# Optimization experiments

Measured on AMD Instinct MI355X. Metric: run time of the kernel, lower is better.

Reference implementation:

```python
import jax, jax.numpy as jnp
import numpy as np

CONNECTIONS = {0: [1, 7], 1: [0, 2], 2: [1, 3], 3: [2], 4: [0, 5], 5: [4, 6], 6: [5], 7: [0, 8], 8: [7, 9, 11, 14], 9: [8, 10], 10: [9], 11: [8, 12], 12: [11, 13], 13: [12], 14: [8, 15], 15: [14, 16], 16: [15]}
J = 17
DIM_IN = 128
DIM_OUT = 128
B, T = 64, 243


def _build_bases():
    A1 = np.zeros((J, J), dtype=np.float32)
    for i, neigh in CONNECTIONS.items():
        for j in neigh:
            A1[i, j] = 1.0
            A1[j, i] = 1.0
    eye = np.eye(J, dtype=np.float32)
    adj1_base = A1 + eye
    paths2 = (A1 @ A1 > 0).astype(np.float32)
    adj2_base = ((paths2 - A1 - eye) > 0).astype(np.float32)
    return jnp.asarray(adj1_base), jnp.asarray(adj2_base)


def setup_inputs() -> dict:
    key = jax.random.key(0)
    ks = jax.random.split(key, 8)
    adj1_base, adj2_base = _build_bases()
    # xavier_uniform with gain 1.414 for W
    bound_w = 1.414 * np.sqrt(6.0 / (DIM_IN + DIM_OUT))
    W = jax.random.uniform(ks[0], (DIM_IN, DIM_OUT), jnp.float32, -bound_w, bound_w)
    bound_b = 1.0 / np.sqrt(DIM_IN)
    b = jax.random.uniform(ks[1], (DIM_OUT,), jnp.float32, -bound_b, bound_b)
    return {
        "x": jax.random.normal(ks[2], (B, T, J, DIM_IN), jnp.float32),
        "W": W,
        "b": b,
        "adj_l1": jnp.zeros((J, J), jnp.float32),
        "adj_l2": jnp.zeros((J, J), jnp.float32),
        "w1": jnp.ones((1,), jnp.float32),
        "w2": jnp.ones((1,), jnp.float32),
        "gate_w": jax.random.normal(ks[3], (DIM_IN, 1), jnp.float32) / np.sqrt(DIM_IN),
        "gate_b": jnp.zeros((1,), jnp.float32),
        "bn_gamma": jnp.ones((DIM_OUT,), jnp.float32),
        "bn_beta": jnp.zeros((DIM_OUT,), jnp.float32),
        "adj1_base": adj1_base,
        "adj2_base": adj2_base,
    }


def reference(x, W, b, adj_l1, adj_l2, w1, w2, gate_w, gate_b, bn_gamma, bn_beta, adj1_base, adj2_base):
    Bb, Tt, Jj, C = x.shape
    xf = x.reshape(Bb * Tt, Jj, C)  # (N, J, C)

    # learnable-weighted static adjacency (symmetrized)
    A1w = adj1_base + jax.nn.sigmoid(adj_l1)
    A2w = adj2_base + jax.nn.sigmoid(adj_l2)
    comb = jax.nn.softplus(w1[0]) * A1w + jax.nn.softplus(w2[0]) * A2w
    comb = 0.5 * (comb + comb.T)  # (J, J)

    # dynamic cosine-similarity adjacency
    nrm = jnp.linalg.norm(xf, axis=-1, keepdims=True)
    xn = xf / jnp.maximum(nrm, 1e-12)
    dyn = jax.nn.relu(jnp.einsum("nic,njc->nij", xn, xn)) + jnp.eye(Jj, dtype=x.dtype)

    gate = jax.nn.sigmoid(xf @ gate_w + gate_b)  # (N, J, 1)
    A = gate * comb[None] + (1.0 - gate) * dyn  # (N, J, J)

    # symmetric degree normalization
    deg = A.sum(-1)  # (N, J)
    d = (deg + 1e-6) ** -0.5
    A_hat = d[:, :, None] * A * d[:, None, :]

    h = jnp.einsum("nij,njc->nic", A_hat, xf @ W) + b  # (N, J, dim_out)

    # BatchNorm1d over channels (training-mode batch stats over N and J)
    mean = h.mean(axis=(0, 1))
    var = h.var(axis=(0, 1))
    h = (h - mean) * jax.lax.rsqrt(var + 1e-5) * bn_gamma + bn_beta

    h = jax.nn.relu(h)
    h = h + xf  # residual (dim_in == dim_out -> identity projection)
    return h.reshape(Bb, Tt, Jj, -1)
```

## Files before the change

### kernel.cpp

```cpp
#include <hip/hip_runtime.h>

typedef unsigned short u16;
typedef unsigned int   u32;
typedef __attribute__((ext_vector_type(8))) short bfrag8;
typedef __attribute__((ext_vector_type(4))) float f32x4;

#define NSAMP  15552
#define GRID_B 3888
#define GRID_G 4131

__device__ __forceinline__ u32 bfr(float f){
  u32 u = __float_as_uint(f);
  return (u + 0x7FFFu + ((u >> 16) & 1u)) >> 16;
}
__device__ __forceinline__ u32 packbf(float lo, float hi){
  return bfr(lo) | (bfr(hi) << 16);
}
__device__ __forceinline__ float ubf(u32 v){ return __uint_as_float(v << 16); }
__device__ __forceinline__ float ubfh(u32 v){ return __uint_as_float(v & 0xFFFF0000u); }
__device__ __forceinline__ float sigm(float v){ return 1.0f / (1.0f + __expf(-v)); }
__device__ __forceinline__ float softp(float v){ return (v > 20.f) ? v : log1pf(__expf(v)); }

__global__ void kA(const float* __restrict__ W, const float* __restrict__ al1,
                   const float* __restrict__ al2, const float* __restrict__ w1,
                   const float* __restrict__ w2, const float* __restrict__ a1b,
                   const float* __restrict__ a2b, u16* __restrict__ wt,
                   float* __restrict__ comb, float* __restrict__ mid){
  int idx = blockIdx.x * 256 + threadIdx.x;
  int k = idx >> 7, n = idx & 127;
  wt[n * 128 + k] = (u16)bfr(W[idx]);
  if (blockIdx.x == 1) mid[threadIdx.x] = 0.f;
  if (blockIdx.x == 0){
    float s1 = softp(w1[0]);
    float s2 = softp(w2[0]);
    for (int p = threadIdx.x; p < 289; p += 256){
      int i = p / 17, j = p - i * 17;
      float mij = s1 * (a1b[i*17+j] + sigm(al1[i*17+j])) + s2 * (a2b[i*17+j] + sigm(al2[i*17+j]));
      float mji = s1 * (a1b[j*17+i] + sigm(al1[j*17+i])) + s2 * (a2b[j*17+i] + sigm(al2[j*17+i]));
      comb[i*20 + j] = 0.5f * (mij + mji);
    }
  }
}

struct __align__(16) QSmem { u16 xb[4][18][136]; };
__global__ __launch_bounds__(256, 4) void kQ(const float* __restrict__ x,
    const float* __restrict__ gw, const float* __restrict__ gb,
    float* __restrict__ gbuf){
  __shared__ QSmem q;
  const int tid = threadIdx.x;
  const int w  = tid >> 6;
  const int l  = tid & 63;
  const int g4 = l >> 4;
  const int lc = l & 15;
  const int s  = blockIdx.x * 4 + w;
  const float* xs = x + (size_t)s * 2176;

  float2 g2 = *(const float2*)(gw + 2*l);
  *(u32*)&q.xb[w][17][2*l] = packbf(g2.x, g2.y);
  #pragma unroll
  for (int j = 0; j < 17; j++){
    float2 v = *(const float2*)(xs + j*128 + 2*l);
    *(u32*)&q.xb[w][j][2*l] = packbf(v.x, v.y);
  }
  __syncthreads();
  __builtin_amdgcn_sched_barrier(0);

  const int rB = 16 + ((lc < 2) ? lc : 1);
  f32x4 z4 = {0.f,0.f,0.f,0.f};
  f32x4 dg00 = z4, dg01 = z4, dg11 = z4;
  #pragma unroll
  for (int ks = 0; ks < 4; ks++){
    const int ko = ks*32 + (g4 << 3);
    bfrag8 a0 = *(const bfrag8*)&q.xb[w][lc][ko];
    bfrag8 a1 = *(const bfrag8*)&q.xb[w][rB][ko];
    dg00 = __builtin_amdgcn_mfma_f32_16x16x32_bf16(a0, a0, dg00, 0,0,0);
    dg01 = __builtin_amdgcn_mfma_f32_16x16x32_bf16(a0, a1, dg01, 0,0,0);
    dg11 = __builtin_amdgcn_mfma_f32_16x16x32_bf16(a1, a1, dg11, 0,0,0);
  }
  float* gs = gbuf + (size_t)s * 384;
  const float gbv = gb[0];
  #pragma unroll
  for (int r = 0; r < 4; r++){
    const int i = (g4 << 2) + r;
    gs[i*20 + lc] = dg00[r];
    if (lc == 0){ gs[i*20 + 16] = dg01[r]; gs[16*20 + i] = dg01[r]; }
    if (lc == 1){ gs[360 + i] = sigm(dg01[r] + gbv); }
  }
  if ((lc >> 2) == g4){
    float v = dg00[lc & 3];
    gs[340 + lc] = 1.0f / fmaxf(sqrtf(v), 1e-12f);
  }
  if (l == 0) gs[340 + 16] = 1.0f / fmaxf(sqrtf(dg11[0]), 1e-12f);
  if (l == 1) gs[360 + 16] = sigm(dg11[0] + gbv);
}

struct WaveMem {
  float G[17][20];
  float scr[64];
};
struct BSmem {
  WaveMem wm[4];
  float   combs[340];
};
static_assert(sizeof(BSmem) <= 81920, "LDS budget");

template<int ZOUT>
__device__ __forceinline__ void kBl_body(
    const float* __restrict__ x, const float* __restrict__ combg,
    const float* __restrict__ gbuf, float* __restrict__ out,
    u16* __restrict__ zbuf){
  __shared__ BSmem sm;
  const int tid = threadIdx.x;
  const int w  = tid >> 6;
  const int l  = tid & 63;
  const int g4 = l >> 4;
  const int lc = l & 15;

  for (int p = tid; p < 340; p += 256) sm.combs[p] = combg[p];

  WaveMem& M = sm.wm[w];
  float* Mf = (float*)&M.G[0][0];
  const int s = blockIdx.x * 4 + w;
  const float* gs = gbuf + (size_t)s * 384;
  for (int p = l; p < 380; p += 64) Mf[p] = gs[p];

  const float* xs = x + (size_t)s * 2176;
  float2 xr[17];
  #pragma unroll
  for (int j = 0; j < 17; j++) xr[j] = *(const float2*)(xs + j*128 + 2*l);
  __syncthreads();

  const float iv16 = M.scr[16], gt16 = M.scr[36];
  const float ivj  = M.scr[lc];
  float av00[4], av01[4], dp0[4];
  #pragma unroll
  for (int r = 0; r < 4; r++){
    const int i0 = (g4 << 2) + r;
    const float iv0 = M.scr[i0], gi0 = M.scr[20 + i0];
    float dyn = (i0 == lc) ? 2.0f : fmaxf(M.G[i0][lc] * iv0 * ivj, 0.f);
    av00[r] = gi0 * sm.combs[i0*20 + lc] + (1.f - gi0) * dyn;
    float dyn16 = fmaxf(M.G[i0][16] * iv0 * iv16, 0.f);
    float a16 = gi0 * sm.combs[i0*20 + 16] + (1.f - gi0) * dyn16;
    av01[r] = (lc == 0) ? a16 : 0.f;
    dp0[r] = av00[r] + av01[r];
  }
  float dyn10 = fmaxf(M.G[16][lc] * iv16 * ivj, 0.f);
  float av10 = gt16 * sm.combs[16*20 + lc] + (1.f - gt16) * dyn10;
  float av11 = (lc == 0) ? (gt16 * sm.combs[16*20 + 16] + (1.f - gt16) * 2.0f) : 0.f;
  float dp1 = av10 + av11;
  #pragma unroll
  for (int m = 1; m <= 8; m <<= 1){
    #pragma unroll
    for (int r = 0; r < 4; r++) dp0[r] += __shfl_xor(dp0[r], m, 64);
    dp1 += __shfl_xor(dp1, m, 64);
  }
  float dd0[4];
  #pragma unroll
  for (int r = 0; r < 4; r++) dd0[r] = rsqrtf(dp0[r] + 1e-6f);
  float dd1 = rsqrtf(dp1 + 1e-6f);
  if (lc == 0){
    #pragma unroll
    for (int r = 0; r < 4; r++) M.scr[40 + (g4<<2) + r] = dd0[r];
  }
  if (l == 0) M.scr[40 + 16] = dd1;
  __syncthreads();

  const float dj0 = M.scr[40 + lc];
  const float dj1 = M.scr[40 + 16];
  #pragma unroll
  for (int r = 0; r < 4; r++){
    const int i0 = (g4 << 2) + r;
    M.G[i0][lc] = dd0[r] * av00[r] * dj0;
    if (lc == 0) M.G[i0][16] = dd0[r] * av01[r] * dj1;
  }
  if (g4 == 0) M.G[16][lc] = dd1 * av10 * dj0;
  if (l == 0)  M.G[16][16] = dd1 * av11 * dj1;
  __syncthreads();

  float* ob = out + (size_t)s * 2176;
  u16*   zb = zbuf + (size_t)s * 2176;
  for (int i = 0; i < 17; i++){
    const float4 a0 = *(const float4*)&M.G[i][0];
    const float4 a1 = *(const float4*)&M.G[i][4];
    const float4 a2 = *(const float4*)&M.G[i][8];
    const float4 a3 = *(const float4*)&M.G[i][12];
    const float a16 = M.G[i][16];
    float zx = a0.x*xr[0].x,  zy = a0.x*xr[0].y;
    zx += a0.y*xr[1].x;  zy += a0.y*xr[1].y;
    zx += a0.z*xr[2].x;  zy += a0.z*xr[2].y;
    zx += a0.w*xr[3].x;  zy += a0.w*xr[3].y;
    zx += a1.x*xr[4].x;  zy += a1.x*xr[4].y;
    zx += a1.y*xr[5].x;  zy += a1.y*xr[5].y;
    zx += a1.z*xr[6].x;  zy += a1.z*xr[6].y;
    zx += a1.w*xr[7].x;  zy += a1.w*xr[7].y;
    zx += a2.x*xr[8].x;  zy += a2.x*xr[8].y;
    zx += a2.y*xr[9].x;  zy += a2.y*xr[9].y;
    zx += a2.z*xr[10].x; zy += a2.z*xr[10].y;
    zx += a2.w*xr[11].x; zy += a2.w*xr[11].y;
    zx += a3.x*xr[12].x; zy += a3.x*xr[12].y;
    zx += a3.y*xr[13].x; zy += a3.y*xr[13].y;
    zx += a3.z*xr[14].x; zy += a3.z*xr[14].y;
    zx += a3.w*xr[15].x; zy += a3.w*xr[15].y;
    zx += a16*xr[16].x;  zy += a16*xr[16].y;
    if (ZOUT == 1){
      *(u32*)&zb[i*128 + 2*l] = packbf(zx, zy);
    } else {
      float2 zv; zv.x = zx; zv.y = zy;
      *(float2*)&ob[i*128 + 2*l] = zv;
    }
  }
}

__global__ __launch_bounds__(256, 4) void kBl2(
    const float* __restrict__ x, const float* __restrict__ combg,
    const float* __restrict__ gbuf, u16* __restrict__ zbuf){
  kBl_body<1>(x, combg, gbuf, nullptr, zbuf);
}
__global__ __launch_bounds__(256, 4) void kBl(
    const float* __restrict__ x, const float* __restrict__ combg,
    const float* __restrict__ gbuf, float* __restrict__ out){
  kBl_body<0>(x, combg, gbuf, out, nullptr);
}

__global__ __launch_bounds__(256, 4) void kBf(
    const float* __restrict__ x, const float* __restrict__ gw,
    const float* __restrict__ gb, const float* __restrict__ combg,
    float* __restrict__ out){
  __shared__ BSmem sm;
  const int tid = threadIdx.x;
  const int w  = tid >> 6;
  const int l  = tid & 63;
  const int g4 = l >> 4;
  const int lc = l & 15;

  for (int p = tid; p < 340; p += 256) sm.combs[p] = combg[p];
  __syncthreads();

  WaveMem& M = sm.wm[w];
  float2 g2 = *(const float2*)(gw + 2*l);
  const float gbv = gb[0];
  const int s = blockIdx.x * 4 + w;
  const float* xs = x + (size_t)s * 2176;
  float2 xr[17];
  #pragma unroll
  for (int j = 0; j < 17; j++) xr[j] = *(const float2*)(xs + j*128 + 2*l);

  #pragma unroll
  for (int i = 0; i < 17; i++){
    float p[17];
    #pragma unroll
    for (int j = i; j < 17; j++)
      p[j-i] = xr[i].x*xr[j].x + xr[i].y*xr[j].y;
    float pg = xr[i].x*g2.x + xr[i].y*g2.y;
    #pragma unroll
    for (int m = 1; m <= 32; m <<= 1){
      #pragma unroll
      for (int j = i; j < 17; j++) p[j-i] += __shfl_xor(p[j-i], m, 64);
      pg += __shfl_xor(pg, m, 64);
    }
    #pragma unroll
    for (int j = i; j < 17; j++){
      if (l == j) M.G[i][j] = p[j-i];
      if (i != j && l == i) M.G[j][i] = p[j-i];
    }
    if (l == i){
      M.scr[i]      = 1.0f / fmaxf(sqrtf(p[0]), 1e-12f);
      M.scr[20 + i] = sigm(pg + gbv);
    }
  }
  __syncthreads();

  const float iv16 = M.scr[16], gt16 = M.scr[36];
  const float ivj  = M.scr[lc];
  float av00[4], av01[4], dp0[4];
  #pragma unroll
  for (int r = 0; r < 4; r++){
    const int i0 = (g4 << 2) + r;
    const float iv0 = M.scr[i0], gi0 = M.scr[20 + i0];
    float dyn = (i0 == lc) ? 2.0f : fmaxf(M.G[i0][lc] * iv0 * ivj, 0.f);
    av00[r] = gi0 * sm.combs[i0*20 + lc] + (1.f - gi0) * dyn;
    float dyn16 = fmaxf(M.G[i0][16] * iv0 * iv16, 0.f);
    float a16 = gi0 * sm.combs[i0*20 + 16] + (1.f - gi0) * dyn16;
    av01[r] = (lc == 0) ? a16 : 0.f;
    dp0[r] = av00[r] + av01[r];
  }
  float dyn10 = fmaxf(M.G[16][lc] * iv16 * ivj, 0.f);
  float av10 = gt16 * sm.combs[16*20 + lc] + (1.f - gt16) * dyn10;
  float av11 = (lc == 0) ? (gt16 * sm.combs[16*20 + 16] + (1.f - gt16) * 2.0f) : 0.f;
  float dp1 = av10 + av11;
  #pragma unroll
  for (int m = 1; m <= 8; m <<= 1){
    #pragma unroll
    for (int r = 0; r < 4; r++) dp0[r] += __shfl_xor(dp0[r], m, 64);
    dp1 += __shfl_xor(dp1, m, 64);
  }
  float dd0[4];
  #pragma unroll
  for (int r = 0; r < 4; r++) dd0[r] = rsqrtf(dp0[r] + 1e-6f);
  float dd1 = rsqrtf(dp1 + 1e-6f);
  if (lc == 0){
    #pragma unroll
    for (int r = 0; r < 4; r++) M.scr[40 + (g4<<2) + r] = dd0[r];
  }
  if (l == 0) M.scr[40 + 16] = dd1;
  __syncthreads();

  const float dj0 = M.scr[40 + lc];
  const float dj1 = M.scr[40 + 16];
  #pragma unroll
  for (int r = 0; r < 4; r++){
    const int i0 = (g4 << 2) + r;
    M.G[i0][lc] = dd0[r] * av00[r] * dj0;
    if (lc == 0) M.G[i0][16] = dd0[r] * av01[r] * dj1;
  }
  if (g4 == 0) M.G[16][lc] = dd1 * av10 * dj0;
  if (l == 0)  M.G[16][16] = dd1 * av11 * dj1;
  __syncthreads();

  float* ob = out + (size_t)s * 2176;
  for (int i = 0; i < 17; i++){
    const float4 a0 = *(const float4*)&M.G[i][0];
    const float4 a1 = *(const float4*)&M.G[i][4];
    const float4 a2 = *(const float4*)&M.G[i][8];
    const float4 a3 = *(const float4*)&M.G[i][12];
    const float a16 = M.G[i][16];
    float zx = a0.x*xr[0].x,  zy = a0.x*xr[0].y;
    zx += a0.y*xr[1].x;  zy += a0.y*xr[1].y;
    zx += a0.z*xr[2].x;  zy += a0.z*xr[2].y;
    zx += a0.w*xr[3].x;  zy += a0.w*xr[3].y;
    zx += a1.x*xr[4].x;  zy += a1.x*xr[4].y;
    zx += a1.y*xr[5].x;  zy += a1.y*xr[5].y;
    zx += a1.z*xr[6].x;  zy += a1.z*xr[6].y;
    zx += a1.w*xr[7].x;  zy += a1.w*xr[7].y;
    zx += a2.x*xr[8].x;  zy += a2.x*xr[8].y;
    zx += a2.y*xr[9].x;  zy += a2.y*xr[9].y;
    zx += a2.z*xr[10].x; zy += a2.z*xr[10].y;
    zx += a2.w*xr[11].x; zy += a2.w*xr[11].y;
    zx += a3.x*xr[12].x; zy += a3.x*xr[12].y;
    zx += a3.y*xr[13].x; zy += a3.y*xr[13].y;
    zx += a3.z*xr[14].x; zy += a3.z*xr[14].y;
    zx += a3.w*xr[15].x; zy += a3.w*xr[15].y;
    zx += a16*xr[16].x;  zy += a16*xr[16].y;
    float2 zv; zv.x = zx; zv.y = zy;
    *(float2*)&ob[i*128 + 2*l] = zv;
  }
}

struct __align__(16) G4Smem {
  float hb[4][16][132];
  float stash[4][256];
};
__global__ __launch_bounds__(256, 4) void kG4(const u16* __restrict__ wtg,
    u16* __restrict__ zbuf, float* __restrict__ part){
  __shared__ G4Smem g;
  const int tid = threadIdx.x;
  const int w  = tid >> 6;
  const int l  = tid & 63;
  const int g4 = l >> 4;
  const int lc = l & 15;
  const int R = blockIdx.x * 64 + w * 16;

  const u16* zr = zbuf + (size_t)R * 128;
  f32x4 zero4 = {0.f,0.f,0.f,0.f};
  f32x4 acc[8];
  #pragma unroll
  for (int nf = 0; nf < 8; nf++) acc[nf] = zero4;
  #pragma unroll
  for (int ks = 0; ks < 4; ks++){
    const int ko = ks*32 + (g4 << 3);
    bfrag8 za = *(const bfrag8*)&zr[lc * 128 + ko];
    #pragma unroll
    for (int nf = 0; nf < 8; nf++){
      bfrag8 bw = *(const bfrag8*)&wtg[(nf*16 + lc)*128 + ko];
      acc[nf] = __builtin_amdgcn_mfma_f32_16x16x32_bf16(za, bw, acc[nf], 0,0,0);
    }
  }

  float s[8], q[8];
  #pragma unroll
  for (int nf = 0; nf < 8; nf++){
    float ss = 0.f, qq = 0.f;
    #pragma unroll
    for (int r = 0; r < 4; r++){
      float v = acc[nf][r];
      g.hb[w][4*g4 + r][nf*16 + lc] = v;
      ss += v; qq += v*v;
    }
    ss += __shfl_xor(ss, 16, 64); ss += __shfl_xor(ss, 32, 64);
    qq += __shfl_xor(qq, 16, 64); qq += __shfl_xor(qq, 32, 64);
    s[nf] = ss; q[nf] = qq;
  }
  __builtin_amdgcn_sched_barrier(0);

  {
    const int row = l >> 2, seg = l & 3;
    const float* hrow = &g.hb[w][row][seg * 32];
    u16* zw = zbuf + (size_t)(R + row) * 128 + seg * 32;
    #pragma unroll
    for (int k = 0; k < 4; k++){
      float4 a = *(const float4*)&hrow[k*8];
      float4 b = *(const float4*)&hrow[k*8 + 4];
      u32 p0 = packbf(a.x, a.y), p1 = packbf(a.z, a.w);
      u32 p2 = packbf(b.x, b.y), p3 = packbf(b.z, b.w);
      uint4 pv; pv.x = p0; pv.y = p1; pv.z = p2; pv.w = p3;
      *(uint4*)&zw[k*8] = pv;
    }
  }

  if (l < 16){
    #pragma unroll
    for (int nf = 0; nf < 8; nf++){
      g.stash[w][nf*16 + l]       = s[nf];
      g.stash[w][128 + nf*16 + l] = q[nf];
    }
  }
  __syncthreads();
  part[(size_t)blockIdx.x * 256 + tid] =
      g.stash[0][tid] + g.stash[1][tid] + g.stash[2][tid] + g.stash[3][tid];
}

__global__ __launch_bounds__(256) void kC(const float* __restrict__ part,
    float* __restrict__ mid){
  __shared__ float smem[256];
  const int t = threadIdx.x, c = blockIdx.x;
  float acc = 0.f;
  for (int g = t; g < GRID_G; g += 256) acc += part[(size_t)g * 256 + c];
  smem[t] = acc;
  __syncthreads();
  for (int sft = 128; sft > 0; sft >>= 1){
    if (t < sft) smem[t] += smem[t + sft];
    __syncthreads();
  }
  if (t == 0) mid[c] = smem[0];
}

__global__ __launch_bounds__(256, 4) void kG2a(const u16* __restrict__ wtg,
    const u16* __restrict__ zbuf, float* __restrict__ mid, float* __restrict__ out){
  __shared__ float stash[4][256];
  const int tid = threadIdx.x;
  const int w  = tid >> 6;
  const int l  = tid & 63;
  const int g4 = l >> 4;
  const int lc = l & 15;
  const int R = blockIdx.x * 64 + w * 16;

  const u16* zr = zbuf + (size_t)R * 128;
  f32x4 zero4 = {0.f,0.f,0.f,0.f};
  f32x4 acc[8];
  #pragma unroll
  for (int nf = 0; nf < 8; nf++) acc[nf] = zero4;
  #pragma unroll
  for (int ks = 0; ks < 4; ks++){
    const int ko = ks*32 + (g4 << 3);
    bfrag8 za = *(const bfrag8*)&zr[lc * 128 + ko];
    #pragma unroll
    for (int nf = 0; nf < 8; nf++){
      bfrag8 bw = *(const bfrag8*)&wtg[(nf*16 + lc)*128 + ko];
      acc[nf] = __builtin_amdgcn_mfma_f32_16x16x32_bf16(za, bw, acc[nf], 0,0,0);
    }
  }
  float* hg = out + (size_t)R * 128;
  float s[8], q[8];
  #pragma unroll
  for (int nf = 0; nf < 8; nf++){
    float ss = 0.f, qq = 0.f;
    #pragma unroll
    for (int r = 0; r < 4; r++){
      float v = acc[nf][r];
      hg[(4*g4 + r)*128 + nf*16 + lc] = v;
      ss += v; qq += v*v;
    }
    ss += __shfl_xor(ss, 16, 64); ss += __shfl_xor(ss, 32, 64);
    qq += __shfl_xor(qq, 16, 64); qq += __shfl_xor(qq, 32, 64);
    s[nf] = ss; q[nf] = qq;
  }
  if (l < 16){
    #pragma unroll
    for (int nf = 0; nf < 8; nf++){
      stash[w][nf*16 + l]       = s[nf];
      stash[w][128 + nf*16 + l] = q[nf];
    }
  }
  __syncthreads();
  atomicAdd(&mid[tid], stash[0][tid] + stash[1][tid] + stash[2][tid] + stash[3][tid]);
}

struct __align__(16) GSmem {
  u16 wl[128][132];
  u16 zl[4][16][132];
};
__global__ __launch_bounds__(256, 3) void kG(const u16* __restrict__ wtg,
    float* __restrict__ mid, float* __restrict__ out){
  __shared__ GSmem g;
  const int tid = threadIdx.x;
  const int w  = tid >> 6;
  const int l  = tid & 63;
  const int g4 = l >> 4;
  const int lc = l & 15;

  for (int p = tid; p < 8192; p += 256){
    int n = p >> 6, k2 = (p & 63) * 2;
    *(u32*)&g.wl[n][k2] = ((const u32*)wtg)[p];
  }
  const int R = blockIdx.x * 64 + w * 16;
  float* zg = out + (size_t)R * 128;
  #pragma unroll
  for (int r = 0; r < 16; r++){
    float2 zv = *(const float2*)&zg[r*128 + 2*l];
    *(u32*)&g.zl[w][r][2*l] = packbf(zv.x, zv.y);
  }
  __syncthreads();
  __builtin_amdgcn_sched_barrier(0);

  f32x4 zero4 = {0.f,0.f,0.f,0.f};
  f32x4 acc[8];
  #pragma unroll
  for (int nf = 0; nf < 8; nf++) acc[nf] = zero4;
  #pragma unroll
  for (int ks = 0; ks < 4; ks++){
    const int ko = ks*32 + (g4 << 3);
    bfrag8 za = *(const bfrag8*)&g.zl[w][lc][ko];
    #pragma unroll
    for (int nf = 0; nf < 8; nf++){
      bfrag8 bw = *(const bfrag8*)&g.wl[nf*16 + lc][ko];
      acc[nf] = __builtin_amdgcn_mfma_f32_16x16x32_bf16(za, bw, acc[nf], 0,0,0);
    }
  }

  float s[8], q[8];
  #pragma unroll
  for (int nf = 0; nf < 8; nf++){
    float ss = 0.f, qq = 0.f;
    #pragma unroll
    for (int r = 0; r < 4; r++){
      float v = acc[nf][r];
      zg[(4*g4 + r)*128 + nf*16 + lc] = v;
      ss += v; qq += v*v;
    }
    ss += __shfl_xor(ss, 16, 64); ss += __shfl_xor(ss, 32, 64);
    qq += __shfl_xor(qq, 16, 64); qq += __shfl_xor(qq, 32, 64);
    s[nf] = ss; q[nf] = qq;
  }

  __syncthreads();
  float* stash = (float*)&g.zl[w][0][0];
  if (l < 16){
    #pragma unroll
    for (int nf = 0; nf < 8; nf++){
      stash[nf*16 + l]       = s[nf];
      stash[128 + nf*16 + l] = q[nf];
    }
  }
  __syncthreads();
  float t0 = ((float*)&g.zl[0][0][0])[tid];
  float t1 = ((float*)&g.zl[1][0][0])[tid];
  float t2 = ((float*)&g.zl[2][0][0])[tid];
  float t3 = ((float*)&g.zl[3][0][0])[tid];
  atomicAdd(&mid[tid], t0 + t1 + t2 + t3);
}

__global__ __launch_bounds__(256) void kD2(const float* __restrict__ x,
    const float* __restrict__ mid, const float* __restrict__ gamma,
    const float* __restrict__ beta, const u16* __restrict__ hbuf,
    float* __restrict__ out){
  __shared__ float sc[128], sh[128];
  const int t = threadIdx.x;
  if (t < 128){
    const float ic = 1.0f / 264384.0f;
    float mean = mid[t] * ic;
    float var  = fmaxf(mid[128 + t] * ic - mean*mean, 0.f);
    float scl  = gamma[t] * rsqrtf(var + 1e-5f);
    sc[t] = scl;
    sh[t] = beta[t] - mean * scl;
  }
  __syncthreads();
  const int total16 = 4230144;
  for (int i = blockIdx.x*256 + t; i < total16; i += 2048*256){
    uint4 hv = ((const uint4*)hbuf)[i];
    float4 x0 = ((const float4*)x)[2*i];
    float4 x1 = ((const float4*)x)[2*i + 1];
    int c0 = (i & 15) << 3;
    float4 r0, r1;
    r0.x = fmaxf(ubf (hv.x)*sc[c0+0] + sh[c0+0], 0.f) + x0.x;
    r0.y = fmaxf(ubfh(hv.x)*sc[c0+1] + sh[c0+1], 0.f) + x0.y;
    r0.z = fmaxf(ubf (hv.y)*sc[c0+2] + sh[c0+2], 0.f) + x0.z;
    r0.w = fmaxf(ubfh(hv.y)*sc[c0+3] + sh[c0+3], 0.f) + x0.w;
    r1.x = fmaxf(ubf (hv.z)*sc[c0+4] + sh[c0+4], 0.f) + x1.x;
    r1.y = fmaxf(ubfh(hv.z)*sc[c0+5] + sh[c0+5], 0.f) + x1.y;
    r1.z = fmaxf(ubf (hv.w)*sc[c0+6] + sh[c0+6], 0.f) + x1.z;
    r1.w = fmaxf(ubfh(hv.w)*sc[c0+7] + sh[c0+7], 0.f) + x1.w;
    ((float4*)out)[2*i]     = r0;
    ((float4*)out)[2*i + 1] = r1;
  }
}

__global__ __launch_bounds__(256) void kD(const float* __restrict__ x,
    const float* __restrict__ mid, const float* __restrict__ gamma,
    const float* __restrict__ beta, float* __restrict__ out){
  __shared__ float sc[128], sh[128];
  const int t = threadIdx.x;
  if (t < 128){
    const float ic = 1.0f / 264384.0f;
    float mean = mid[t] * ic;
    float var  = fmaxf(mid[128 + t] * ic - mean*mean, 0.f);
    float scl  = gamma[t] * rsqrtf(var + 1e-5f);
    sc[t] = scl;
    sh[t] = beta[t] - mean * scl;
  }
  __syncthreads();
  const int total = 8460288;
  for (int i = blockIdx.x*256 + t; i < total; i += 2048*256){
    float4 h  = ((const float4*)out)[i];
    float4 xv = ((const float4*)x)[i];
    int c0 = (i & 31) << 2;
    float4 r;
    r.x = fmaxf(h.x*sc[c0+0] + sh[c0+0], 0.f) + xv.x;
    r.y = fmaxf(h.y*sc[c0+1] + sh[c0+1], 0.f) + xv.y;
    r.z = fmaxf(h.z*sc[c0+2] + sh[c0+2], 0.f) + xv.z;
    r.w = fmaxf(h.w*sc[c0+3] + sh[c0+3], 0.f) + xv.w;
    ((float4*)out)[i] = r;
  }
}

extern "C" void kernel_launch(void* const* d_in, const int* in_sizes, int n_in,
                              void* d_out, int out_size, void* d_ws, size_t ws_size,
                              hipStream_t stream){
  (void)in_sizes; (void)n_in; (void)out_size;
  const float* x     = (const float*)d_in[0];
  const float* W     = (const float*)d_in[1];
  const float* al1   = (const float*)d_in[3];
  const float* al2   = (const float*)d_in[4];
  const float* w1    = (const float*)d_in[5];
  const float* w2    = (const float*)d_in[6];
  const float* gw    = (const float*)d_in[7];
  const float* gb    = (const float*)d_in[8];
  const float* gamma = (const float*)d_in[9];
  const float* beta  = (const float*)d_in[10];
  const float* a1b   = (const float*)d_in[11];
  const float* a2b   = (const float*)d_in[12];
  float* out = (float*)d_out;

  float* wsf  = (float*)d_ws;
  float* comb = wsf;
  u16*   wt   = (u16*)(wsf + 384);
  float* mid  = wsf + 384 + 8192;
  float* gbuf = wsf + 384 + 8192 + 256;
  u16*   zbuf = (u16*)(gbuf + (size_t)NSAMP*384);
  float* part = (float*)(zbuf + (size_t)NSAMP*2176);
  const size_t base  = (size_t)(384 + 8192 + 256) * 4;
  const size_t need1 = base + (size_t)NSAMP*384*4;
  const size_t need2 = need1 + (size_t)NSAMP*2176*2;
  const size_t need3 = need2 + (size_t)GRID_G*256*4;

  hipLaunchKernelGGL(kA, dim3(64), dim3(256), 0, stream, W, al1, al2, w1, w2, a1b, a2b, wt, comb, mid);
  if (ws_size >= need3){
    hipLaunchKernelGGL(kQ,   dim3(GRID_B), dim3(256), 0, stream, x, gw, gb, gbuf);
    hipLaunchKernelGGL(kBl2, dim3(GRID_B), dim3(256), 0, stream, x, comb, gbuf, zbuf);
    hipLaunchKernelGGL(kG4,  dim3(GRID_G), dim3(256), 0, stream, wt, zbuf, part);
    hipLaunchKernelGGL(kC,   dim3(256),    dim3(256), 0, stream, part, mid);
    hipLaunchKernelGGL(kD2,  dim3(2048),   dim3(256), 0, stream, x, mid, gamma, beta, zbuf, out);
  } else if (ws_size >= need2){
    hipLaunchKernelGGL(kQ,   dim3(GRID_B), dim3(256), 0, stream, x, gw, gb, gbuf);
    hipLaunchKernelGGL(kBl2, dim3(GRID_B), dim3(256), 0, stream, x, comb, gbuf, zbuf);
    hipLaunchKernelGGL(kG2a, dim3(GRID_G), dim3(256), 0, stream, wt, zbuf, mid, out);
    hipLaunchKernelGGL(kD,   dim3(2048),   dim3(256), 0, stream, x, mid, gamma, beta, out);
  } else if (ws_size >= need1){
    hipLaunchKernelGGL(kQ,  dim3(GRID_B), dim3(256), 0, stream, x, gw, gb, gbuf);
    hipLaunchKernelGGL(kBl, dim3(GRID_B), dim3(256), 0, stream, x, comb, gbuf, out);
    hipLaunchKernelGGL(kG,  dim3(GRID_G), dim3(256), 0, stream, wt, mid, out);
    hipLaunchKernelGGL(kD,  dim3(2048),   dim3(256), 0, stream, x, mid, gamma, beta, out);
  } else {
    hipLaunchKernelGGL(kBf, dim3(GRID_B), dim3(256), 0, stream, x, gw, gb, comb, out);
    hipLaunchKernelGGL(kG,  dim3(GRID_G), dim3(256), 0, stream, wt, mid, out);
    hipLaunchKernelGGL(kD,  dim3(2048),   dim3(256), 0, stream, x, mid, gamma, beta, out);
  }
}
```

Baseline: 225.7 us.

## Make GEMM kernel persistent over tiles with prefetched Z fragments

Replaces the one-tile-per-wave GEMM kernel with a version where each wave loops over 8 consecutive 16-row tiles. It prefetches the next tile's Z fragments while computing the current one, and accumulates BatchNorm partial sums across tiles in registers. This cuts the grid from 4131 to 517 blocks and shrinks the partial-sum array that the reduction kernel reads. The risk is fewer blocks (517) and lower occupancy, which may underfill the GPU and expose latency.

```diff
diff --git a/kernel.cpp b/kernel.cpp
--- a/kernel.cpp
+++ b/kernel.cpp
@@ -8,6 +8,8 @@
 #define NSAMP  15552
 #define GRID_B 3888
 #define GRID_G 4131
+#define NTILE  16524
+#define GRID_G7 517
 
 __device__ __forceinline__ u32 bfr(float f){
   u32 u = __float_as_uint(f);
@@ -346,67 +348,97 @@
   }
 }
 
-struct __align__(16) G4Smem {
+struct __align__(16) G7Smem {
   float hb[4][16][132];
   float stash[4][256];
 };
-__global__ __launch_bounds__(256, 4) void kG4(const u16* __restrict__ wtg,
+__global__ __launch_bounds__(256, 3) void kG7(const u16* __restrict__ wtg,
     u16* __restrict__ zbuf, float* __restrict__ part){
-  __shared__ G4Smem g;
+  __shared__ G7Smem g;
   const int tid = threadIdx.x;
   const int w  = tid >> 6;
   const int l  = tid & 63;
   const int g4 = l >> 4;
   const int lc = l & 15;
-  const int R = blockIdx.x * 64 + w * 16;
-
-  const u16* zr = zbuf + (size_t)R * 128;
-  f32x4 zero4 = {0.f,0.f,0.f,0.f};
-  f32x4 acc[8];
-  #pragma unroll
-  for (int nf = 0; nf < 8; nf++) acc[nf] = zero4;
-  #pragma unroll
-  for (int ks = 0; ks < 4; ks++){
-    const int ko = ks*32 + (g4 << 3);
-    bfrag8 za = *(const bfrag8*)&zr[lc * 128 + ko];
+  const int row = l >> 2, seg = l & 3;
+  const int tb = blockIdx.x * 32 + w * 8;
+
+  float s[8], q[8];
+  #pragma unroll
+  for (int nf = 0; nf < 8; nf++){ s[nf] = 0.f; q[nf] = 0.f; }
+
+  bfrag8 zf[4], zn[4];
+  if (tb < NTILE){
+    const u16* zr = zbuf + (size_t)tb * 2048;
+    #pragma unroll
+    for (int ks = 0; ks < 4; ks++)
+      zf[ks] = *(const bfrag8*)&zr[lc*128 + ks*32 + (g4 << 3)];
+  }
+
+  for (int t = 0; t < 8; ++t){
+    const int tile = tb + t;
+    if (tile >= NTILE) break;
+    if (t < 7 && tile + 1 < NTILE){
+      const u16* zr = zbuf + (size_t)(tile + 1) * 2048;
+      #pragma unroll
+      for (int ks = 0; ks < 4; ks++)
+        zn[ks] = *(const bfrag8*)&zr[lc*128 + ks*32 + (g4 << 3)];
+    }
+
+    f32x4 zero4 = {0.f,0.f,0.f,0.f};
+    f32x4 acc[8];
+    #pragma unroll
+    for (int nf = 0; nf < 8; nf++) acc[nf] = zero4;
     #pragma unroll
     for (int nf = 0; nf < 8; nf++){
-      bfrag8 bw = *(const bfrag8*)&wtg[(nf*16 + lc)*128 + ko];
-      acc[nf] = __builtin_amdgcn_mfma_f32_16x16x32_bf16(za, bw, acc[nf], 0,0,0);
-    }
-  }
-
-  float s[8], q[8];
+      const u16* wr = &wtg[(nf*16 + lc)*128 + (g4 << 3)];
+      bfrag8 w0 = *(const bfrag8*)&wr[0];
+      bfrag8 w1 = *(const bfrag8*)&wr[32];
+      bfrag8 w2 = *(const bfrag8*)&wr[64];
+      bfrag8 w3 = *(const bfrag8*)&wr[96];
+      acc[nf] = __builtin_amdgcn_mfma_f32_16x16x32_bf16(zf[0], w0, acc[nf], 0,0,0);
+      acc[nf] = __builtin_amdgcn_mfma_f32_16x16x32_bf16(zf[1], w1, acc[nf], 0,0,0);
+      acc[nf] = __builtin_amdgcn_mfma_f32_16x16x32_bf16(zf[2], w2, acc[nf], 0,0,0);
+      acc[nf] = __builtin_amdgcn_mfma_f32_16x16x32_bf16(zf[3], w3, acc[nf], 0,0,0);
+    }
+
+    #pragma unroll
+    for (int nf = 0; nf < 8; nf++){
+      #pragma unroll
+      for (int r = 0; r < 4; r++){
+        float v = acc[nf][r];
+        g.hb[w][4*g4 + r][nf*16 + lc] = v;
+        s[nf] += v; q[nf] += v*v;
+      }
+    }
+    __builtin_amdgcn_sched_barrier(0);
+
+    {
+      const float* hrow = &g.hb[w][row][seg * 32];
+      u16* zw = zbuf + ((size_t)tile * 16 + row) * 128 + seg * 32;
+      #pragma unroll
+      for (int k = 0; k < 4; k++){
+        float4 a = *(const float4*)&hrow[k*8];
+        float4 b = *(const float4*)&hrow[k*8 + 4];
+        uint4 pv;
+        pv.x = packbf(a.x, a.y); pv.y = packbf(a.z, a.w);
+        pv.z = packbf(b.x, b.y); pv.w = packbf(b.z, b.w);
+        *(uint4*)&zw[k*8] = pv;
+      }
+    }
+    __builtin_amdgcn_sched_barrier(0);
+
+    if (t < 7){
+      #pragma unroll
+      for (int ks = 0; ks < 4; ks++) zf[ks] = zn[ks];
+    }
+  }
+
   #pragma unroll
   for (int nf = 0; nf < 8; nf++){
-    float ss = 0.f, qq = 0.f;
-    #pragma unroll
-    for (int r = 0; r < 4; r++){
-      float v = acc[nf][r];
-      g.hb[w][4*g4 + r][nf*16 + lc] = v;
-      ss += v; qq += v*v;
-    }
-    ss += __shfl_xor(ss, 16, 64); ss += __shfl_xor(ss, 32, 64);
-    qq += __shfl_xor(qq, 16, 64); qq += __shfl_xor(qq, 32, 64);
-    s[nf] = ss; q[nf] = qq;
-  }
-  __builtin_amdgcn_sched_barrier(0);
-
-  {
-    const int row = l >> 2, seg = l & 3;
-    const float* hrow = &g.hb[w][row][seg * 32];
-    u16* zw = zbuf + (size_t)(R + row) * 128 + seg * 32;
-    #pragma unroll
-    for (int k = 0; k < 4; k++){
-      float4 a = *(const float4*)&hrow[k*8];
-      float4 b = *(const float4*)&hrow[k*8 + 4];
-      u32 p0 = packbf(a.x, a.y), p1 = packbf(a.z, a.w);
-      u32 p2 = packbf(b.x, b.y), p3 = packbf(b.z, b.w);
-      uint4 pv; pv.x = p0; pv.y = p1; pv.z = p2; pv.w = p3;
-      *(uint4*)&zw[k*8] = pv;
-    }
-  }
-
+    s[nf] += __shfl_xor(s[nf], 16, 64); s[nf] += __shfl_xor(s[nf], 32, 64);
+    q[nf] += __shfl_xor(q[nf], 16, 64); q[nf] += __shfl_xor(q[nf], 32, 64);
+  }
   if (l < 16){
     #pragma unroll
     for (int nf = 0; nf < 8; nf++){
@@ -420,11 +452,11 @@
 }
 
 __global__ __launch_bounds__(256) void kC(const float* __restrict__ part,
-    float* __restrict__ mid){
+    float* __restrict__ mid, int nblk){
   __shared__ float smem[256];
   const int t = threadIdx.x, c = blockIdx.x;
   float acc = 0.f;
-  for (int g = t; g < GRID_G; g += 256) acc += part[(size_t)g * 256 + c];
+  for (int g = t; g < nblk; g += 256) acc += part[(size_t)g * 256 + c];
   smem[t] = acc;
   __syncthreads();
   for (int sft = 128; sft > 0; sft >>= 1){
@@ -654,11 +686,11 @@
 
   hipLaunchKernelGGL(kA, dim3(64), dim3(256), 0, stream, W, al1, al2, w1, w2, a1b, a2b, wt, comb, mid);
   if (ws_size >= need3){
-    hipLaunchKernelGGL(kQ,   dim3(GRID_B), dim3(256), 0, stream, x, gw, gb, gbuf);
-    hipLaunchKernelGGL(kBl2, dim3(GRID_B), dim3(256), 0, stream, x, comb, gbuf, zbuf);
-    hipLaunchKernelGGL(kG4,  dim3(GRID_G), dim3(256), 0, stream, wt, zbuf, part);
-    hipLaunchKernelGGL(kC,   dim3(256),    dim3(256), 0, stream, part, mid);
-    hipLaunchKernelGGL(kD2,  dim3(2048),   dim3(256), 0, stream, x, mid, gamma, beta, zbuf, out);
+    hipLaunchKernelGGL(kQ,   dim3(GRID_B),  dim3(256), 0, stream, x, gw, gb, gbuf);
+    hipLaunchKernelGGL(kBl2, dim3(GRID_B),  dim3(256), 0, stream, x, comb, gbuf, zbuf);
+    hipLaunchKernelGGL(kG7,  dim3(GRID_G7), dim3(256), 0, stream, wt, zbuf, part);
+    hipLaunchKernelGGL(kC,   dim3(256),     dim3(256), 0, stream, part, mid, GRID_G7);
+    hipLaunchKernelGGL(kD2,  dim3(2048),    dim3(256), 0, stream, x, mid, gamma, beta, zbuf, out);
   } else if (ws_size >= need2){
     hipLaunchKernelGGL(kQ,   dim3(GRID_B), dim3(256), 0, stream, x, gw, gb, gbuf);
     hipLaunchKernelGGL(kBl2, dim3(GRID_B), dim3(256), 0, stream, x, comb, gbuf, zbuf);
```

Result: slower. 251.0 us (+11.2%).
